# Performance work log

Hardware: AMD Instinct MI355X
Metric: run time of the kernel (lower is better)

## Reference

```python
import jax, jax.numpy as jnp
import numpy as np

B, S, HID = 2, 8192, 1024
NH, DH, CL = 16, 64, 128
NB, NA = 1, 0  # num_chunks_before, num_chunks_after
NC = S // CL
MASK_VALUE = -1e9


def _look_adjacent(v):
    # v: [..., n_chunks, chunk_len(*d)] with chunk axis=2; torch's
    # cat([v[:,:,i:], v[:,:,:i]], dim=2) == jnp.roll(v, -i, axis=2)
    slices = [jnp.roll(v, -i, axis=2) for i in range(-NB, NA + 1)]
    return jnp.concatenate(slices, axis=3)


def setup_inputs() -> dict:
    key = jax.random.key(0)
    k1, k2, k3, k4 = jax.random.split(key, 4)
    scale = 1.0 / np.sqrt(HID).astype(np.float32)
    hidden_states = jax.random.normal(k1, (B, S, HID), jnp.float32)
    Wq = jax.random.normal(k2, (HID, NH * DH), jnp.float32) * scale
    Wk = jax.random.normal(k3, (HID, NH * DH), jnp.float32) * scale
    Wv = jax.random.normal(k4, (HID, NH * DH), jnp.float32) * scale
    return {"hidden_states": hidden_states, "Wq": Wq, "Wk": Wk, "Wv": Wv}


def _forward(hidden_states, Wq, Wk, Wv):
    # project and split heads -> [B, NH, NC, CL, DH]
    def proj(W):
        x = (hidden_states @ W).reshape(B, S, NH, DH)
        return x.transpose(0, 2, 1, 3).reshape(B, NH, NC, CL, DH)

    q = proj(Wq)
    k = proj(Wk) / jnp.sqrt(jnp.asarray(DH, hidden_states.dtype))
    v = proj(Wv)

    k_adj = _look_adjacent(k)  # [B, NH, NC, (NB+1+NA)*CL, DH]
    v_adj = _look_adjacent(v)

    # per-chunk scores: [B, NH, NC, CL, (NB+1+NA)*CL]
    dots = jnp.einsum("bhnqd,bhnkd->bhnqk", q, k_adj)

    # causal mask via position indices (decoder). Chunk 0's wrapped-around
    # keys carry large indices and are correctly masked out.
    idx = jnp.arange(S).reshape(1, 1, NC, CL)
    kv_idx = _look_adjacent(idx)  # [1, 1, NC, (NB+1+NA)*CL]
    causal = idx[..., :, None] >= kv_idx[..., None, :]
    dots = jnp.where(causal, dots, jnp.asarray(MASK_VALUE, dots.dtype))

    probs = jax.nn.softmax(dots, axis=-1)
    out = jnp.einsum("bhnqk,bhnkd->bhnqd", probs, v_adj)
    # merge chunks and heads -> [B, S, NH*DH]
    out = out.reshape(B, NH, S, DH).transpose(0, 2, 1, 3).reshape(B, S, NH * DH)
    return out


def reference(hidden_states, Wq, Wk, Wv):
    return _forward(hidden_states, Wq, Wk, Wv)
```

## Files before the change

kernel.cpp:

```cpp
#include <hip/hip_runtime.h>
#include <stdint.h>


typedef unsigned short u16;
typedef __bf16 bf16x8 __attribute__((ext_vector_type(8)));
typedef float f32x4 __attribute__((ext_vector_type(4)));

typedef __attribute__((address_space(1))) void* gas_ptr;
typedef __attribute__((address_space(3))) void* las_ptr;

__device__ __forceinline__ u16 f2bf(float f) {
  uint32_t u = __float_as_uint(f);
  u += 0x7fffu + ((u >> 16) & 1u);
  return (u16)(u >> 16);
}

__device__ __forceinline__ void gload16(const void* g, void* l) {
  __builtin_amdgcn_global_load_lds((gas_ptr)g, (las_ptr)l, 16, 0, 0);
}

__global__ void k_conv_x(const float* __restrict__ x, u16* __restrict__ o, int n4) {
  int i = blockIdx.x * blockDim.x + threadIdx.x;
  int stride = gridDim.x * blockDim.x;
  for (; i < n4; i += stride) {
    float4 v = reinterpret_cast<const float4*>(x)[i];
    unsigned long long pk = (unsigned long long)f2bf(v.x) |
                            ((unsigned long long)f2bf(v.y) << 16) |
                            ((unsigned long long)f2bf(v.z) << 32) |
                            ((unsigned long long)f2bf(v.w) << 48);
    reinterpret_cast<unsigned long long*>(o)[i] = pk;
  }
}

__global__ void k_conv_w(const float* __restrict__ wq, const float* __restrict__ wk,
                         const float* __restrict__ wv, u16* __restrict__ wt) {
  __shared__ float tile[32][33];
  int z = blockIdx.z;
  const float* src = (z == 0) ? wq : (z == 1) ? wk : wv;
  float scale = (z == 1) ? 0.125f : 1.0f;
  int n0 = blockIdx.x * 32, k0 = blockIdx.y * 32;
  int tx = threadIdx.x, ty = threadIdx.y;
  for (int i = ty; i < 32; i += 8)
    tile[i][tx] = src[(size_t)(k0 + i) * 1024 + n0 + tx];
  __syncthreads();
  u16* dst = wt + (size_t)z * 1024 * 1024;
  for (int i = ty; i < 32; i += 8)
    dst[(size_t)(n0 + i) * 1024 + k0 + tx] = f2bf(tile[tx][i] * scale);
}

template <int TR_OUT>
__global__ __launch_bounds__(256, 2) void k_gemm(const u16* __restrict__ xb,
                                                 const u16* __restrict__ wt,
                                                 u16* __restrict__ out) {
  __shared__ __align__(16) char lds[32768];
  char* a_s = lds;
  char* b_s = lds + 16384;
  const int tid = threadIdx.x;
  const int lane = tid & 63, l16 = lane & 15, lhi = lane >> 4;
  const int wave = tid >> 6;
  const int wm = (wave >> 1) * 64, wn = (wave & 1) * 64;
  const int m0 = blockIdx.y * 128, n0 = blockIdx.x * 128;
  const int dstb = (tid & 192) * 16;

  f32x4 acc[4][4] = {};

  for (int kt = 0; kt < 16; ++kt) {
    __syncthreads();
#pragma unroll
    for (int it = 0; it < 4; ++it) {
      int idx = it * 256 + tid;
      int row = idx >> 3;
      int colb = (idx & 7) * 16;
      int scol = colb ^ ((row & 7) << 4);
      gload16((const char*)xb + ((size_t)(m0 + row) * 1024 + kt * 64) * 2 + scol,
              a_s + it * 4096 + dstb);
      gload16((const char*)wt + ((size_t)(n0 + row) * 1024 + kt * 64) * 2 + scol,
              b_s + it * 4096 + dstb);
    }
    __syncthreads();
#pragma unroll
    for (int ks = 0; ks < 2; ++ks) {
      bf16x8 af[4], bf[4];
#pragma unroll
      for (int rb = 0; rb < 4; ++rb) {
        int row = wm + rb * 16 + l16;
        af[rb] = *(const bf16x8*)(a_s + row * 128 + ((ks * 64 + lhi * 16) ^ ((row & 7) << 4)));
      }
#pragma unroll
      for (int nb = 0; nb < 4; ++nb) {
        int row = wn + nb * 16 + l16;
        bf[nb] = *(const bf16x8*)(b_s + row * 128 + ((ks * 64 + lhi * 16) ^ ((row & 7) << 4)));
      }
#pragma unroll
      for (int rb = 0; rb < 4; ++rb) {
#pragma unroll
        for (int nb = 0; nb < 4; ++nb) {
          if constexpr (TR_OUT)
            acc[rb][nb] = __builtin_amdgcn_mfma_f32_16x16x32_bf16(af[rb], bf[nb], acc[rb][nb], 0, 0, 0);
          else
            acc[rb][nb] = __builtin_amdgcn_mfma_f32_16x16x32_bf16(bf[nb], af[rb], acc[rb][nb], 0, 0, 0);
        }
      }
    }
  }

  if constexpr (!TR_OUT) {
#pragma unroll
    for (int rb = 0; rb < 4; ++rb) {
#pragma unroll
      for (int nb = 0; nb < 4; ++nb) {
        int m = m0 + wm + rb * 16 + l16;
        int n = n0 + wn + nb * 16 + lhi * 4;
        unsigned long long pk = (unsigned long long)f2bf(acc[rb][nb][0]) |
                                ((unsigned long long)f2bf(acc[rb][nb][1]) << 16) |
                                ((unsigned long long)f2bf(acc[rb][nb][2]) << 32) |
                                ((unsigned long long)f2bf(acc[rb][nb][3]) << 48);
        *(unsigned long long*)((char*)out + ((size_t)m * 1024 + n) * 2) = pk;
      }
    }
  } else {
#pragma unroll
    for (int rb = 0; rb < 4; ++rb) {
#pragma unroll
      for (int nb = 0; nb < 4; ++nb) {
        int m = m0 + wm + rb * 16 + lhi * 4;
        int n = n0 + wn + nb * 16 + l16;
        int bb = m >> 13;
        int s = m & 8191;
        unsigned long long pk = (unsigned long long)f2bf(acc[rb][nb][0]) |
                                ((unsigned long long)f2bf(acc[rb][nb][1]) << 16) |
                                ((unsigned long long)f2bf(acc[rb][nb][2]) << 32) |
                                ((unsigned long long)f2bf(acc[rb][nb][3]) << 48);
        *(unsigned long long*)((char*)out + ((size_t)(bb * 1024 + n) * 8192 + s) * 2) = pk;
      }
    }
  }
}

__global__ __launch_bounds__(256, 2) void k_attn(const u16* __restrict__ qw,
                                                 const u16* __restrict__ kw,
                                                 const u16* __restrict__ vt,
                                                 float* __restrict__ out) {
  __shared__ __align__(16) char lds[81920];
  char* q_s = lds;
  char* k_s = lds + 16384;
  char* v_s = lds + 49152;
  const int tid = threadIdx.x;
  const int lane = tid & 63, l16 = lane & 15, lhi = lane >> 4;
  const int wave = tid >> 6;
  char* p_s = lds + wave * 8192;
  const int c = blockIdx.x & 63;
  const int h = (blockIdx.x >> 6) & 15;
  const int b = blockIdx.x >> 10;
  const int cprev = (c == 0) ? 0 : c - 1;
  const int dstb = (tid & 192) * 16;

#pragma unroll
  for (int it = 0; it < 4; ++it) {
    int idx = it * 256 + tid;
    int row = idx >> 3, colb = (idx & 7) * 16;
    gload16((const char*)qw + ((size_t)(b * 8192 + c * 128 + row) * 1024 + h * 64) * 2 +
                (colb ^ ((row & 7) << 4)),
            q_s + it * 4096 + dstb);
  }
#pragma unroll
  for (int it = 0; it < 8; ++it) {
    int idx = it * 256 + tid;
    int row = idx >> 3, colb = (idx & 7) * 16;
    int srow = (row < 128) ? (cprev * 128 + row) : (c * 128 + row - 128);
    gload16((const char*)kw + ((size_t)(b * 8192 + srow) * 1024 + h * 64) * 2 +
                (colb ^ ((row & 7) << 4)),
            k_s + it * 4096 + dstb);
  }
#pragma unroll
  for (int it = 0; it < 8; ++it) {
    int idx = it * 256 + tid;
    int row = idx >> 5;
    int colb = (idx & 31) * 16;
    int colbl = colb ^ ((row & 7) << 4);
    size_t roff = ((size_t)((b * 16 + h) * 64 + row)) * 8192 * 2;
    size_t soff = c ? ((size_t)(c * 128 - 128) * 2 + colbl) : (size_t)(colbl & 255);
    gload16((const char*)vt + roff + soff, v_s + it * 4096 + dstb);
  }
  __syncthreads();

  const int rbase = wave * 32;
  f32x4 accs[2][16];
#pragma unroll
  for (int rb = 0; rb < 2; ++rb)
#pragma unroll
    for (int nb = 0; nb < 16; ++nb) accs[rb][nb] = f32x4{0.f, 0.f, 0.f, 0.f};

#pragma unroll
  for (int ks = 0; ks < 2; ++ks) {
    bf16x8 af[2];
#pragma unroll
    for (int rb = 0; rb < 2; ++rb) {
      int row = rbase + rb * 16 + l16;
      af[rb] = *(const bf16x8*)(q_s + row * 128 + ((ks * 64 + lhi * 16) ^ ((row & 7) << 4)));
    }
#pragma unroll
    for (int nb = 0; nb < 16; ++nb) {
      int row = nb * 16 + l16;
      bf16x8 bfb = *(const bf16x8*)(k_s + row * 128 + ((ks * 64 + lhi * 16) ^ ((row & 7) << 4)));
#pragma unroll
      for (int rb = 0; rb < 2; ++rb)
        accs[rb][nb] = __builtin_amdgcn_mfma_f32_16x16x32_bf16(af[rb], bfb, accs[rb][nb], 0, 0, 0);
    }
  }

  float rinv[2][4];
#pragma unroll
  for (int rb = 0; rb < 2; ++rb) {
#pragma unroll
    for (int j = 0; j < 4; ++j) {
      int qi = rbase + rb * 16 + lhi * 4 + j;
      float m = -3.0e38f;
#pragma unroll
      for (int nb = 0; nb < 16; ++nb) {
        int kl = nb * 16 + l16;
        float v = accs[rb][nb][j];
        bool valid = (kl <= qi + 128) && ((c > 0) || (kl >= 128));
        v = valid ? v : -1.0e9f;
        accs[rb][nb][j] = v;
        m = fmaxf(m, v);
      }
#pragma unroll
      for (int d = 1; d < 16; d <<= 1) m = fmaxf(m, __shfl_xor(m, d));
      float s = 0.f;
#pragma unroll
      for (int nb = 0; nb < 16; ++nb) {
        float e = __expf(accs[rb][nb][j] - m);
        accs[rb][nb][j] = e;
        s += e;
      }
#pragma unroll
      for (int d = 1; d < 16; d <<= 1) s += __shfl_xor(s, d);
      rinv[rb][j] = 1.0f / s;
    }
  }

  __syncthreads();

  f32x4 acco[2][4] = {};
#pragma unroll
  for (int half = 0; half < 2; ++half) {
#pragma unroll
    for (int rb = 0; rb < 2; ++rb) {
#pragma unroll
      for (int nbh = 0; nbh < 8; ++nbh) {
#pragma unroll
        for (int j = 0; j < 4; ++j) {
          int r = rb * 16 + lhi * 4 + j;
          int cb = (nbh * 16 + l16) * 2;
          *(u16*)(p_s + r * 256 + (cb ^ ((r & 7) << 4))) = f2bf(accs[rb][half * 8 + nbh][j]);
        }
      }
    }
    __asm__ volatile("s_waitcnt lgkmcnt(0)" ::: "memory");
    __builtin_amdgcn_sched_barrier(0);
#pragma unroll
    for (int ks = 0; ks < 4; ++ks) {
      bf16x8 pf[2];
#pragma unroll
      for (int rb = 0; rb < 2; ++rb) {
        int r = rb * 16 + l16;
        pf[rb] = *(const bf16x8*)(p_s + r * 256 + ((ks * 64 + lhi * 16) ^ ((r & 7) << 4)));
      }
#pragma unroll
      for (int db = 0; db < 4; ++db) {
        int vr = db * 16 + l16;
        bf16x8 vf = *(const bf16x8*)(v_s + vr * 512 +
                                     ((half * 256 + ks * 64 + lhi * 16) ^ ((vr & 7) << 4)));
#pragma unroll
        for (int rb = 0; rb < 2; ++rb)
          acco[rb][db] = __builtin_amdgcn_mfma_f32_16x16x32_bf16(pf[rb], vf, acco[rb][db], 0, 0, 0);
      }
    }
    if (half == 0) {
      __asm__ volatile("s_waitcnt lgkmcnt(0)" ::: "memory");
      __builtin_amdgcn_sched_barrier(0);
    }
  }

#pragma unroll
  for (int rb = 0; rb < 2; ++rb) {
#pragma unroll
    for (int db = 0; db < 4; ++db) {
#pragma unroll
      for (int j = 0; j < 4; ++j) {
        int r = rbase + rb * 16 + lhi * 4 + j;
        out[(size_t)(b * 8192 + c * 128 + r) * 1024 + h * 64 + db * 16 + l16] =
            acco[rb][db][j] * rinv[rb][j];
      }
    }
  }
}

extern "C" void kernel_launch(void* const* d_in, const int* in_sizes, int n_in,
                              void* d_out, int out_size, void* d_ws, size_t ws_size,
                              hipStream_t stream) {
  const float* hs = (const float*)d_in[0];
  const float* wq = (const float*)d_in[1];
  const float* wk = (const float*)d_in[2];
  const float* wv = (const float*)d_in[3];
  float* out = (float*)d_out;
  char* ws = (char*)d_ws;

  u16* x_bf = (u16*)ws;
  u16* wt   = (u16*)(ws + 33554432);
  u16* q_ws = (u16*)(ws + 39845888);
  u16* k_ws = (u16*)(ws + 73400320);
  u16* v_t  = (u16*)(ws + 106954752);

  k_conv_x<<<dim3(2048), dim3(256), 0, stream>>>(hs, x_bf, 16384 * 1024 / 4);
  k_conv_w<<<dim3(32, 32, 3), dim3(32, 8), 0, stream>>>(wq, wk, wv, wt);
  k_gemm<0><<<dim3(8, 128), dim3(256), 0, stream>>>(x_bf, wt, q_ws);
  k_gemm<0><<<dim3(8, 128), dim3(256), 0, stream>>>(x_bf, wt + 1024 * 1024, k_ws);
  k_gemm<1><<<dim3(8, 128), dim3(256), 0, stream>>>(x_bf, wt + 2 * 1024 * 1024, v_t);
  k_attn<<<dim3(2048), dim3(256), 0, stream>>>(q_ws, k_ws, v_t, out);
}
```

Before: 327.7 us.

## Rewrite projection GEMM with 256x256 tiles and double-buffered LDS prefetch

Replaces the 128x128 single-buffered GEMM with a 512-thread, 256x256-tile kernel that double-buffers A and B in 128KB LDS. Loads for the next k-step are issued in quarter phases interleaved with MFMA work. Explicit waitcnt, barriers and setprio control the overlap, and a block-index swizzle groups blocks for L2 reuse. The 256-block grid leaves little room for waves on 256 CUs, and the large LDS footprint limits occupancy to one block per CU.

```diff
diff --git a/kernel.cpp b/kernel.cpp
--- a/kernel.cpp
+++ b/kernel.cpp
@@ -49,88 +49,128 @@
 }
 
 template <int TR_OUT>
-__global__ __launch_bounds__(256, 2) void k_gemm(const u16* __restrict__ xb,
+__global__ __launch_bounds__(512, 2) void k_gemm(const u16* __restrict__ xb,
                                                  const u16* __restrict__ wt,
                                                  u16* __restrict__ out) {
-  __shared__ __align__(16) char lds[32768];
-  char* a_s = lds;
-  char* b_s = lds + 16384;
+  __shared__ __align__(16) char lds[131072];
+  char* As = lds;
+  char* Bs = lds + 65536;
   const int tid = threadIdx.x;
   const int lane = tid & 63, l16 = lane & 15, lhi = lane >> 4;
   const int wave = tid >> 6;
-  const int wm = (wave >> 1) * 64, wn = (wave & 1) * 64;
-  const int m0 = blockIdx.y * 128, n0 = blockIdx.x * 128;
-  const int dstb = (tid & 192) * 16;
-
-  f32x4 acc[4][4] = {};
-
-  for (int kt = 0; kt < 16; ++kt) {
-    __syncthreads();
-#pragma unroll
-    for (int it = 0; it < 4; ++it) {
-      int idx = it * 256 + tid;
-      int row = idx >> 3;
-      int colb = (idx & 7) * 16;
-      int scol = colb ^ ((row & 7) << 4);
-      gload16((const char*)xb + ((size_t)(m0 + row) * 1024 + kt * 64) * 2 + scol,
-              a_s + it * 4096 + dstb);
-      gload16((const char*)wt + ((size_t)(n0 + row) * 1024 + kt * 64) * 2 + scol,
-              b_s + it * 4096 + dstb);
-    }
-    __syncthreads();
-#pragma unroll
-    for (int ks = 0; ks < 2; ++ks) {
-      bf16x8 af[4], bf[4];
-#pragma unroll
-      for (int rb = 0; rb < 4; ++rb) {
-        int row = wm + rb * 16 + l16;
-        af[rb] = *(const bf16x8*)(a_s + row * 128 + ((ks * 64 + lhi * 16) ^ ((row & 7) << 4)));
-      }
-#pragma unroll
-      for (int nb = 0; nb < 4; ++nb) {
-        int row = wn + nb * 16 + l16;
-        bf[nb] = *(const bf16x8*)(b_s + row * 128 + ((ks * 64 + lhi * 16) ^ ((row & 7) << 4)));
-      }
-#pragma unroll
-      for (int rb = 0; rb < 4; ++rb) {
-#pragma unroll
-        for (int nb = 0; nb < 4; ++nb) {
-          if constexpr (TR_OUT)
-            acc[rb][nb] = __builtin_amdgcn_mfma_f32_16x16x32_bf16(af[rb], bf[nb], acc[rb][nb], 0, 0, 0);
-          else
-            acc[rb][nb] = __builtin_amdgcn_mfma_f32_16x16x32_bf16(bf[nb], af[rb], acc[rb][nb], 0, 0, 0);
-        }
-      }
+  const int wm = (wave >> 2) * 128;
+  const int wn = (wave & 3) * 64;
+  const int bid = blockIdx.x;
+  const int wg = (bid & 7) * 32 + (bid >> 3);
+  const int m0 = (wg >> 2) * 256;
+  const int n0 = (wg & 3) * 256;
+
+  const int lrow8 = lane >> 3;
+  const int scolx = ((lane & 7) * 16) ^ (lrow8 << 4);
+
+  f32x4 acc[8][4] = {};
+
+  auto stA = [&](int buf, int kt, int h) {
+#pragma unroll
+    for (int i = 0; i < 2; ++i) {
+      int j = wave * 2 + i;
+      int rb = 8 * j + 64 * (h + (j >> 3));
+      int row = rb + lrow8;
+      gload16((const char*)xb + ((size_t)(m0 + row) * 1024 + kt * 64) * 2 + scolx,
+              As + buf * 32768 + rb * 128);
+    }
+  };
+  auto stB = [&](int buf, int kt, int h) {
+#pragma unroll
+    for (int i = 0; i < 2; ++i) {
+      int j = wave * 2 + i;
+      int rb = 8 * (j & 3) + (j >> 2) * 64 + h * 32;
+      int row = rb + lrow8;
+      gload16((const char*)wt + ((size_t)(n0 + row) * 1024 + kt * 64) * 2 + scolx,
+              Bs + buf * 32768 + rb * 128);
+    }
+  };
+
+  stA(0, 0, 0); stB(0, 0, 0); stA(0, 0, 1); stB(0, 0, 1);
+
+  for (int t = 0; t < 16; ++t) {
+    const int cbuf = t & 1, nbuf = cbuf ^ 1;
+    const int ktn = (t < 15) ? t + 1 : 15;
+#pragma unroll
+    for (int p = 0; p < 4; ++p) {
+      __builtin_amdgcn_sched_barrier(0);
+      if (p < 3) asm volatile("s_waitcnt vmcnt(4)" ::: "memory");
+      __builtin_amdgcn_s_barrier();
+      __builtin_amdgcn_sched_barrier(0);
+      const int mh = p & 1, nh = p >> 1;
+      bf16x8 af[4][2], bfr[2][2];
+#pragma unroll
+      for (int fi = 0; fi < 4; ++fi) {
+        int row = wm + (mh * 4 + fi) * 16 + l16;
+#pragma unroll
+        for (int ks = 0; ks < 2; ++ks)
+          af[fi][ks] = *(const bf16x8*)(As + cbuf * 32768 + row * 128 +
+                                        ((ks * 64 + lhi * 16) ^ ((row & 7) << 4)));
+      }
+#pragma unroll
+      for (int f2 = 0; f2 < 2; ++f2) {
+        int rn = wn + nh * 32 + f2 * 16 + l16;
+#pragma unroll
+        for (int ks = 0; ks < 2; ++ks)
+          bfr[f2][ks] = *(const bf16x8*)(Bs + cbuf * 32768 + rn * 128 +
+                                         ((ks * 64 + lhi * 16) ^ ((rn & 7) << 4)));
+      }
+      if (p == 0) stA(nbuf, ktn, 0);
+      else if (p == 1) stB(nbuf, ktn, 0);
+      else if (p == 2) stA(nbuf, ktn, 1);
+      else stB(nbuf, ktn, 1);
+      asm volatile("s_waitcnt lgkmcnt(0)" ::: "memory");
+      __builtin_amdgcn_sched_barrier(0);
+      __builtin_amdgcn_s_setprio(1);
+#pragma unroll
+      for (int fi = 0; fi < 4; ++fi)
+#pragma unroll
+        for (int f2 = 0; f2 < 2; ++f2)
+#pragma unroll
+          for (int ks = 0; ks < 2; ++ks) {
+            if constexpr (TR_OUT)
+              acc[mh * 4 + fi][nh * 2 + f2] = __builtin_amdgcn_mfma_f32_16x16x32_bf16(
+                  af[fi][ks], bfr[f2][ks], acc[mh * 4 + fi][nh * 2 + f2], 0, 0, 0);
+            else
+              acc[mh * 4 + fi][nh * 2 + f2] = __builtin_amdgcn_mfma_f32_16x16x32_bf16(
+                  bfr[f2][ks], af[fi][ks], acc[mh * 4 + fi][nh * 2 + f2], 0, 0, 0);
+          }
+      __builtin_amdgcn_s_setprio(0);
     }
   }
 
   if constexpr (!TR_OUT) {
 #pragma unroll
-    for (int rb = 0; rb < 4; ++rb) {
-#pragma unroll
-      for (int nb = 0; nb < 4; ++nb) {
-        int m = m0 + wm + rb * 16 + l16;
-        int n = n0 + wn + nb * 16 + lhi * 4;
-        unsigned long long pk = (unsigned long long)f2bf(acc[rb][nb][0]) |
-                                ((unsigned long long)f2bf(acc[rb][nb][1]) << 16) |
-                                ((unsigned long long)f2bf(acc[rb][nb][2]) << 32) |
-                                ((unsigned long long)f2bf(acc[rb][nb][3]) << 48);
+    for (int fr = 0; fr < 8; ++fr) {
+#pragma unroll
+      for (int fn = 0; fn < 4; ++fn) {
+        int m = m0 + wm + fr * 16 + l16;
+        int n = n0 + wn + fn * 16 + lhi * 4;
+        unsigned long long pk = (unsigned long long)f2bf(acc[fr][fn][0]) |
+                                ((unsigned long long)f2bf(acc[fr][fn][1]) << 16) |
+                                ((unsigned long long)f2bf(acc[fr][fn][2]) << 32) |
+                                ((unsigned long long)f2bf(acc[fr][fn][3]) << 48);
         *(unsigned long long*)((char*)out + ((size_t)m * 1024 + n) * 2) = pk;
       }
     }
   } else {
 #pragma unroll
-    for (int rb = 0; rb < 4; ++rb) {
-#pragma unroll
-      for (int nb = 0; nb < 4; ++nb) {
-        int m = m0 + wm + rb * 16 + lhi * 4;
-        int n = n0 + wn + nb * 16 + l16;
+    for (int fr = 0; fr < 8; ++fr) {
+#pragma unroll
+      for (int fn = 0; fn < 4; ++fn) {
+        int m = m0 + wm + fr * 16 + lhi * 4;
+        int n = n0 + wn + fn * 16 + l16;
         int bb = m >> 13;
         int s = m & 8191;
-        unsigned long long pk = (unsigned long long)f2bf(acc[rb][nb][0]) |
-                                ((unsigned long long)f2bf(acc[rb][nb][1]) << 16) |
-                                ((unsigned long long)f2bf(acc[rb][nb][2]) << 32) |
-                                ((unsigned long long)f2bf(acc[rb][nb][3]) << 48);
+        unsigned long long pk = (unsigned long long)f2bf(acc[fr][fn][0]) |
+                                ((unsigned long long)f2bf(acc[fr][fn][1]) << 16) |
+                                ((unsigned long long)f2bf(acc[fr][fn][2]) << 32) |
+                                ((unsigned long long)f2bf(acc[fr][fn][3]) << 48);
         *(unsigned long long*)((char*)out + ((size_t)(bb * 1024 + n) * 8192 + s) * 2) = pk;
       }
     }
@@ -315,8 +355,8 @@
 
   k_conv_x<<<dim3(2048), dim3(256), 0, stream>>>(hs, x_bf, 16384 * 1024 / 4);
   k_conv_w<<<dim3(32, 32, 3), dim3(32, 8), 0, stream>>>(wq, wk, wv, wt);
-  k_gemm<0><<<dim3(8, 128), dim3(256), 0, stream>>>(x_bf, wt, q_ws);
-  k_gemm<0><<<dim3(8, 128), dim3(256), 0, stream>>>(x_bf, wt + 1024 * 1024, k_ws);
-  k_gemm<1><<<dim3(8, 128), dim3(256), 0, stream>>>(x_bf, wt + 2 * 1024 * 1024, v_t);
+  k_gemm<0><<<dim3(256), dim3(512), 0, stream>>>(x_bf, wt, q_ws);
+  k_gemm<0><<<dim3(256), dim3(512), 0, stream>>>(x_bf, wt + 1024 * 1024, k_ws);
+  k_gemm<1><<<dim3(256), dim3(512), 0, stream>>>(x_bf, wt + 2 * 1024 * 1024, v_t);
   k_attn<<<dim3(2048), dim3(256), 0, stream>>>(q_ws, k_ws, v_t, out);
 }
```

New measurement: 297.0 us. -9.4%, faster.
